# Optimization experiments

Measured on AMD Instinct MI355X. Metric: run time of the kernel, lower is better.

Reference implementation:

```python
import jax, jax.numpy as jnp
import numpy as np

HEADS = 8
WINDOW = 16

def _pointwise(W, b, t):
    # Conv1d(C, C, kernel=1): (B, C, T) -> (B, C, T)
    return jnp.einsum('oc,bct->bot', W, t) + b[None, :, None]

def setup_inputs() -> dict:
    key = jax.random.key(0)
    ks = jax.random.split(key, 10)
    B, C, T = 4, 512, 4096
    s = 0.02
    return {
        'x':    jax.random.normal(ks[0], (B, C, T), jnp.float32),
        'cond': jax.random.normal(ks[1], (B, C, T), jnp.float32),
        'Wq': jax.random.normal(ks[2], (C, C), jnp.float32) * s,
        'bq': jnp.zeros((C,), jnp.float32),
        'Wk': jax.random.normal(ks[3], (C, C), jnp.float32) * s,
        'bk': jnp.zeros((C,), jnp.float32),
        'Wv': jax.random.normal(ks[4], (C, C), jnp.float32) * s,
        'bv': jnp.zeros((C,), jnp.float32),
        'Wo': jax.random.normal(ks[5], (C, C), jnp.float32) * s,
        'bo': jnp.zeros((C,), jnp.float32),
    }

def reference(x, cond, Wq, bq, Wk, bk, Wv, bv, Wo, bo):
    B, C, T = x.shape
    H, W = HEADS, WINDOW
    hd = C // H
    scale = hd ** (-0.5)
    pad_left = W // 2          # 8
    pad_right = W - pad_left - 1  # 7

    q = _pointwise(Wq, bq, x)      # (B, C, T)
    k = _pointwise(Wk, bk, cond)
    v = _pointwise(Wv, bv, cond)

    k = jnp.pad(k, ((0, 0), (0, 0), (pad_left, pad_right)))  # (B, C, T+W-1)
    v = jnp.pad(v, ((0, 0), (0, 0), (pad_left, pad_right)))

    # sliding windows of size W, stride 1 -> T_unf == T
    idx = jnp.arange(T)[:, None] + jnp.arange(W)[None, :]  # (T, W)
    k_win = k[:, :, idx].reshape(B, H, hd, T, W)
    v_win = v[:, :, idx].reshape(B, H, hd, T, W)
    qh = q.reshape(B, H, hd, T)

    dots = jnp.einsum('bhdt,bhdtw->bhtw', qh, k_win) * scale
    attn = jax.nn.softmax(dots, axis=-1)
    out = jnp.einsum('bhtw,bhdtw->bhdt', attn, v_win)  # (B, H, hd, T)
    out = out.reshape(B, C, T)
    return _pointwise(Wo, bo, out)
```

## Files before the change

kernel.cpp:

```cpp
#include <hip/hip_runtime.h>

#define CC 512
#define TT 4096
#define NB 4
#define NH 8
#define HD 64

typedef __attribute__((ext_vector_type(8))) short s16x8;
typedef __attribute__((ext_vector_type(4))) float f32x4;
typedef __attribute__((ext_vector_type(4))) unsigned int u32x4;
typedef __attribute__((ext_vector_type(2))) unsigned int u32x2;

__device__ __forceinline__ short f2bf(float f) {
    unsigned u = __float_as_uint(f);
    unsigned r = (u + 0x7fffu + ((u >> 16) & 1u)) >> 16;
    return (short)r;
}
__device__ __forceinline__ unsigned pkbf(float a, float b) {
    return (unsigned)(unsigned short)f2bf(a) | ((unsigned)(unsigned short)f2bf(b) << 16);
}

__device__ __forceinline__ void gld_lds16(const void* g, void* s) {
    __builtin_amdgcn_global_load_lds(
        (const __attribute__((address_space(1))) unsigned int*)g,
        (__attribute__((address_space(3))) unsigned int*)s, 16, 0, 0);
}

__global__ __launch_bounds__(256) void cvt_w_k(const float* __restrict__ w0,
                                               const float* __restrict__ w1,
                                               const float* __restrict__ w2,
                                               const float* __restrict__ w3,
                                               short* __restrict__ dst) {
    int i = blockIdx.x * 256 + threadIdx.x;
    const float* s = (i < 262144) ? w0 : (i < 524288) ? w1 : (i < 786432) ? w2 : w3;
    dst[i] = f2bf(s[i & 262143]);
}

__global__ __launch_bounds__(256) void trans_k(const float* __restrict__ x,
                                               const float* __restrict__ cond,
                                               short* __restrict__ xT,
                                               short* __restrict__ condT) {
    __shared__ float tile[64][65];
    int z = blockIdx.z;
    int b = z & 3;
    const float* src = (z < 4 ? x : cond) + (size_t)b * CC * TT;
    short* dst = (z < 4 ? xT : condT) + (size_t)b * TT * CC;
    int tx = threadIdx.x & 63, ty = threadIdx.x >> 6;
    int t0 = blockIdx.x * 64, c0 = blockIdx.y * 64;
#pragma unroll
    for (int r = 0; r < 64; r += 4)
        tile[ty + r][tx] = src[(size_t)(c0 + ty + r) * TT + t0 + tx];
    __syncthreads();
#pragma unroll
    for (int r = 0; r < 64; r += 4)
        dst[(size_t)(t0 + ty + r) * CC + c0 + tx] = f2bf(tile[tx][ty + r]);
}

template <int OMODE>
__device__ __forceinline__ void gemm128(const short* __restrict__ Wm,
                                        const short* __restrict__ Sm,
                                        const float* __restrict__ bias,
                                        float* __restrict__ Df,
                                        short* __restrict__ Db) {
    __shared__ short Al[128 * 64] __attribute__((aligned(16)));
    __shared__ short Bl[128 * 64] __attribute__((aligned(16)));
    const int tid = threadIdx.x;
    const int lane = tid & 63;
    const int wid = tid >> 6;
    const int o0 = blockIdx.y * 128;
    const int t0 = blockIdx.x * 128;
    const int wm = (wid >> 1) * 64;
    const int wn = (wid & 1) * 64;

    f32x4 acc[4][4];
#pragma unroll
    for (int i = 0; i < 4; i++)
#pragma unroll
        for (int j = 0; j < 4; j++) acc[i][j] = (f32x4){0.f, 0.f, 0.f, 0.f};

    const int cbase = (wid * 4) << 6;

    for (int kt = 0; kt < 8; ++kt) {
        const int k0 = kt * 64;
        __syncthreads();
#pragma unroll
        for (int j = 0; j < 4; ++j) {
            int c = cbase + (j << 6) + lane;
            int m = c >> 3, kc = c & 7;
            int kcs = kc ^ (m & 7);
            gld_lds16(Wm + (size_t)(o0 + m) * CC + k0 + kcs * 8,
                      &Al[(cbase + (j << 6)) << 3]);
            gld_lds16(Sm + (size_t)(t0 + m) * CC + k0 + kcs * 8,
                      &Bl[(cbase + (j << 6)) << 3]);
        }
        __syncthreads();
#pragma unroll
        for (int kk = 0; kk < 2; ++kk) {
            const int kb = kk * 32 + (lane >> 4) * 8;
            s16x8 af[4], bfr[4];
#pragma unroll
            for (int i = 0; i < 4; i++) {
                int m = wm + i * 16 + (lane & 15);
                af[i] = *(const s16x8*)&Al[(m * 64 + kb) ^ ((m & 7) << 3)];
                int n = wn + i * 16 + (lane & 15);
                bfr[i] = *(const s16x8*)&Bl[(n * 64 + kb) ^ ((n & 7) << 3)];
            }
#pragma unroll
            for (int mi = 0; mi < 4; mi++)
#pragma unroll
                for (int ni = 0; ni < 4; ni++) {
                    if (OMODE == 1)
                        acc[mi][ni] = __builtin_amdgcn_mfma_f32_16x16x32_bf16(
                            bfr[mi], af[ni], acc[mi][ni], 0, 0, 0);
                    else
                        acc[mi][ni] = __builtin_amdgcn_mfma_f32_16x16x32_bf16(
                            af[mi], bfr[ni], acc[mi][ni], 0, 0, 0);
                }
        }
    }

    const int col = lane & 15;
    const int rg = (lane >> 4) << 2;
    if (OMODE == 1) {
#pragma unroll
        for (int ti = 0; ti < 4; ti++) {
            int t = t0 + wn + ti * 16 + rg;
#pragma unroll
            for (int oi = 0; oi < 4; oi++) {
                int o = o0 + wm + oi * 16 + col;
                float bv = bias[o];
                f32x4 a = acc[ti][oi];
#pragma unroll
                for (int r = 0; r < 4; r++)
                    Db[(size_t)(t + r) * CC + o] = f2bf(a[r] + bv);
            }
        }
    } else {
#pragma unroll
        for (int mi = 0; mi < 4; mi++) {
            int o = o0 + wm + mi * 16 + rg;
#pragma unroll
            for (int ni = 0; ni < 4; ni++) {
                int t = t0 + wn + ni * 16 + col;
                f32x4 a = acc[mi][ni];
#pragma unroll
                for (int r = 0; r < 4; r++) {
                    if (OMODE == 0)
                        Df[(size_t)(o + r) * TT + t] = a[r] + bias[o + r];
                    else
                        Db[(size_t)(o + r) * TT + t] = f2bf(a[r] + bias[o + r]);
                }
            }
        }
    }
}

__global__ __launch_bounds__(256, 2) void gemm_qkv_k(
    const short* __restrict__ Wb, const short* __restrict__ xT,
    const short* __restrict__ condT, const float* __restrict__ bq,
    const float* __restrict__ bk, const float* __restrict__ bv,
    short* __restrict__ qkvT) {
    int z = blockIdx.z, which = z >> 2, b = z & 3;
    const short* Wm = Wb + (size_t)which * CC * CC;
    const short* Sm = (which == 0 ? xT : condT) + (size_t)b * TT * CC;
    short* Db = qkvT + ((size_t)which * NB + b) * TT * CC;
    if (which == 2)
        gemm128<2>(Wm, Sm, bv, nullptr, Db);
    else
        gemm128<1>(Wm, Sm, which == 0 ? bq : bk, nullptr, Db);
}

__global__ __launch_bounds__(256, 2) void gemm_o_k(const short* __restrict__ Wb,
                                                   const short* __restrict__ outT,
                                                   const float* __restrict__ bo,
                                                   float* __restrict__ out) {
    int b = blockIdx.z;
    gemm128<0>(Wb + 3 * (size_t)CC * CC, outT + (size_t)b * TT * CC, bo,
               out + (size_t)b * CC * TT, nullptr);
}

__global__ __launch_bounds__(64, 4) void attn6_k(const short* __restrict__ qkvT,
                                                 short* __restrict__ outT) {
    __shared__ unsigned P_lds[2][16][18];
    const int lane = threadIdx.x;
    const int g = lane >> 4, tp = lane & 15;
    const int T0 = blockIdx.x * 32;
    const int h = blockIdx.y, b = blockIdx.z;
    const size_t BTC = (size_t)NB * TT * CC;
    const short* qg = qkvT + (size_t)b * TT * CC + h * HD;
    const short* kg = qg + BTC;
    const short* vg = qkvT + 2 * BTC + (size_t)b * TT * CC + (size_t)(h * HD) * TT;
    const f32x4 z4 = {0.f, 0.f, 0.f, 0.f};

    s16x8 ka0, ka1;
    {
        int s = T0 - 8 + tp;
        s = s < 0 ? 0 : s;
        const short* p = &kg[(size_t)s * CC + g * 8];
        ka0 = *(const s16x8*)p;
        ka1 = *(const s16x8*)(p + 32);
    }

#pragma unroll
    for (int m = 0; m < 2; ++m) {
        const int sb0 = T0 + 16 * m - 8;
        s16x8 kb0, kb1;
        {
            int s = sb0 + 16 + tp;
            s = s > TT - 1 ? TT - 1 : s;
            const short* p = &kg[(size_t)s * CC + g * 8];
            kb0 = *(const s16x8*)p;
            kb1 = *(const s16x8*)(p + 32);
        }
        s16x8 q0, q1;
        {
            const short* p = &qg[(size_t)(T0 + 16 * m + tp) * CC + g * 8];
            q0 = *(const s16x8*)p;
            q1 = *(const s16x8*)(p + 32);
        }
        int cb = sb0 + g * 8;
        cb = cb < 0 ? 0 : (cb > TT - 8 ? TT - 8 : cb);
        const short* vrow = &vg[(size_t)tp * TT + cb];
        s16x8 vf0 = *(const s16x8*)(vrow);
        s16x8 vf1 = *(const s16x8*)(vrow + (size_t)16 * TT);
        s16x8 vf2 = *(const s16x8*)(vrow + (size_t)32 * TT);
        s16x8 vf3 = *(const s16x8*)(vrow + (size_t)48 * TT);

        f32x4 s0 = __builtin_amdgcn_mfma_f32_16x16x32_bf16(ka0, q0, z4, 0, 0, 0);
        s0 = __builtin_amdgcn_mfma_f32_16x16x32_bf16(ka1, q1, s0, 0, 0, 0);
        f32x4 s1 = __builtin_amdgcn_mfma_f32_16x16x32_bf16(kb0, q0, z4, 0, 0, 0);
        s1 = __builtin_amdgcn_mfma_f32_16x16x32_bf16(kb1, q1, s1, 0, 0, 0);

        float lg[8];
        float mymax = -3.0e38f;
#pragma unroll
        for (int jr = 0; jr < 8; ++jr) {
            const int j = jr >> 2, r = jr & 3;
            float v = (j ? s1[r] : s0[r]) * 0.125f;
            const int sl = 16 * j + 4 * g + r;
            const int sg = sb0 + sl;
            v = ((unsigned)sg < (unsigned)TT) ? v : 0.f;
            lg[jr] = v;
            const bool inw = (unsigned)(sl - tp) < 16u;
            mymax = inw ? fmaxf(mymax, v) : mymax;
        }
        mymax = fmaxf(mymax, __shfl_xor(mymax, 16));
        mymax = fmaxf(mymax, __shfl_xor(mymax, 32));
        float e[8], Z = 0.f;
#pragma unroll
        for (int jr = 0; jr < 8; ++jr) {
            const int j = jr >> 2, r = jr & 3;
            const int sl = 16 * j + 4 * g + r;
            const bool inw = (unsigned)(sl - tp) < 16u;
            const float ee = inw ? __expf(lg[jr] - mymax) : 0.f;
            e[jr] = ee;
            Z += ee;
        }
        Z += __shfl_xor(Z, 16);
        Z += __shfl_xor(Z, 32);
        const float inv = 1.f / Z;
#pragma unroll
        for (int jr = 0; jr < 8; ++jr) {
            const int sg = sb0 + 16 * (jr >> 2) + 4 * g + (jr & 3);
            e[jr] = ((unsigned)sg < (unsigned)TT) ? e[jr] * inv : 0.f;
        }

        unsigned* prow = &P_lds[m & 1][tp][0];
        *(u32x2*)&prow[2 * g] = (u32x2){pkbf(e[0], e[1]), pkbf(e[2], e[3])};
        *(u32x2*)&prow[8 + 2 * g] = (u32x2){pkbf(e[4], e[5]), pkbf(e[6], e[7])};
        __syncthreads();
        const s16x8 pf = *(const s16x8*)&P_lds[m & 1][tp][4 * g];

        f32x4 o0 = __builtin_amdgcn_mfma_f32_16x16x32_bf16(vf0, pf, z4, 0, 0, 0);
        f32x4 o1 = __builtin_amdgcn_mfma_f32_16x16x32_bf16(vf1, pf, z4, 0, 0, 0);
        f32x4 o2 = __builtin_amdgcn_mfma_f32_16x16x32_bf16(vf2, pf, z4, 0, 0, 0);
        f32x4 o3 = __builtin_amdgcn_mfma_f32_16x16x32_bf16(vf3, pf, z4, 0, 0, 0);

        short* orow = &outT[((size_t)b * TT + T0 + 16 * m + tp) * CC + h * HD + 4 * g];
        *(u32x2*)&orow[0] = (u32x2){pkbf(o0[0], o0[1]), pkbf(o0[2], o0[3])};
        *(u32x2*)&orow[16] = (u32x2){pkbf(o1[0], o1[1]), pkbf(o1[2], o1[3])};
        *(u32x2*)&orow[32] = (u32x2){pkbf(o2[0], o2[1]), pkbf(o2[2], o2[3])};
        *(u32x2*)&orow[48] = (u32x2){pkbf(o3[0], o3[1]), pkbf(o3[2], o3[3])};

        ka0 = kb0;
        ka1 = kb1;
    }
}

extern "C" void kernel_launch(void* const* d_in, const int* in_sizes, int n_in,
                              void* d_out, int out_size, void* d_ws, size_t ws_size,
                              hipStream_t stream) {
    const float* x    = (const float*)d_in[0];
    const float* cond = (const float*)d_in[1];
    const float* Wq   = (const float*)d_in[2];
    const float* bq   = (const float*)d_in[3];
    const float* Wk   = (const float*)d_in[4];
    const float* bk   = (const float*)d_in[5];
    const float* Wv   = (const float*)d_in[6];
    const float* bv   = (const float*)d_in[7];
    const float* Wo   = (const float*)d_in[8];
    const float* bo   = (const float*)d_in[9];

    char* ws = (char*)d_ws;
    short* Wb    = (short*)ws;
    short* xT    = (short*)(ws + (2u << 20));
    short* condT = (short*)(ws + (18u << 20));
    short* qkvT  = (short*)(ws + (34u << 20));
    short* outT  = xT;

    cvt_w_k<<<4096, 256, 0, stream>>>(Wq, Wk, Wv, Wo, Wb);
    trans_k<<<dim3(TT / 64, CC / 64, 8), 256, 0, stream>>>(x, cond, xT, condT);
    gemm_qkv_k<<<dim3(TT / 128, CC / 128, 12), 256, 0, stream>>>(Wb, xT, condT, bq, bk, bv, qkvT);
    attn6_k<<<dim3(TT / 32, NH, NB), 64, 0, stream>>>(qkvT, outT);
    gemm_o_k<<<dim3(TT / 128, CC / 128, 4), 256, 0, stream>>>(Wb, outT, bo, (float*)d_out);
}
```

Before: 96.27 us.

## Enlarge GEMM tile to 256x128, load weights directly to registers, double-buffer activations

The shared GEMM routine now computes a 256-row output-channel by 128-token tile per block, with each wave owning a 128x64 sub-tile. Weight fragments are read from global memory straight into registers instead of being staged in LDS, on the expectation that the small weight matrix stays cached. The activation tile is double-buffered in LDS so the next K slice loads while MFMAs run on the current one, which drops one barrier per iteration. The trade-off is more accumulator registers per thread, half as many blocks in the grid, and uncoalesced per-lane global loads for the weights.

```diff
diff --git a/kernel.cpp b/kernel.cpp
--- a/kernel.cpp
+++ b/kernel.cpp
@@ -57,79 +57,92 @@
 }
 
 template <int OMODE>
-__device__ __forceinline__ void gemm128(const short* __restrict__ Wm,
+__device__ __forceinline__ void gemm256(const short* __restrict__ Wm,
                                         const short* __restrict__ Sm,
                                         const float* __restrict__ bias,
                                         float* __restrict__ Df,
                                         short* __restrict__ Db) {
-    __shared__ short Al[128 * 64] __attribute__((aligned(16)));
-    __shared__ short Bl[128 * 64] __attribute__((aligned(16)));
+    __shared__ short Bl[2][128 * 64] __attribute__((aligned(16)));
     const int tid = threadIdx.x;
     const int lane = tid & 63;
     const int wid = tid >> 6;
-    const int o0 = blockIdx.y * 128;
+    const int o0 = blockIdx.y * 256;
     const int t0 = blockIdx.x * 128;
-    const int wm = (wid >> 1) * 64;
+    const int wm = (wid >> 1) * 128;
     const int wn = (wid & 1) * 64;
 
-    f32x4 acc[4][4];
-#pragma unroll
-    for (int i = 0; i < 4; i++)
+    f32x4 acc[8][4];
+#pragma unroll
+    for (int i = 0; i < 8; i++)
 #pragma unroll
         for (int j = 0; j < 4; j++) acc[i][j] = (f32x4){0.f, 0.f, 0.f, 0.f};
 
-    const int cbase = (wid * 4) << 6;
+#define STAGE_B(BUF, K0)                                                     \
+    {                                                                        \
+        _Pragma("unroll") for (int it = 0; it < 4; ++it) {                   \
+            int idx = it * 256 + tid;                                        \
+            int row = idx >> 3, sl = idx & 7;                                \
+            int c = sl ^ (row & 7);                                          \
+            gld_lds16(Sm + (size_t)(t0 + row) * CC + (K0) + c * 8,           \
+                      &Bl[BUF][idx * 8]);                                    \
+        }                                                                    \
+    }
+
+    STAGE_B(0, 0);
+    __syncthreads();
 
     for (int kt = 0; kt < 8; ++kt) {
         const int k0 = kt * 64;
+        const int buf = kt & 1;
+
+        s16x8 af[2][8];
+        const short* abase =
+            Wm + (size_t)(o0 + wm + (lane & 15)) * CC + k0 + (lane >> 4) * 8;
+#pragma unroll
+        for (int ai = 0; ai < 8; ++ai) {
+            af[0][ai] = *(const s16x8*)(abase + (size_t)ai * 16 * CC);
+            af[1][ai] = *(const s16x8*)(abase + (size_t)ai * 16 * CC + 32);
+        }
+
+        if (kt < 7) STAGE_B(buf ^ 1, k0 + 64);
+
+#pragma unroll
+        for (int kk = 0; kk < 2; ++kk) {
+            s16x8 bfr[4];
+#pragma unroll
+            for (int bi = 0; bi < 4; ++bi) {
+                int n = wn + bi * 16 + (lane & 15);
+                bfr[bi] = *(const s16x8*)&Bl[buf][(n * 64 + kk * 32 +
+                                                   (lane >> 4) * 8) ^
+                                                  ((n & 7) << 3)];
+            }
+#pragma unroll
+            for (int ai = 0; ai < 8; ++ai)
+#pragma unroll
+                for (int bi = 0; bi < 4; ++bi) {
+                    if (OMODE == 1)
+                        acc[ai][bi] = __builtin_amdgcn_mfma_f32_16x16x32_bf16(
+                            bfr[bi], af[kk][ai], acc[ai][bi], 0, 0, 0);
+                    else
+                        acc[ai][bi] = __builtin_amdgcn_mfma_f32_16x16x32_bf16(
+                            af[kk][ai], bfr[bi], acc[ai][bi], 0, 0, 0);
+                }
+        }
         __syncthreads();
-#pragma unroll
-        for (int j = 0; j < 4; ++j) {
-            int c = cbase + (j << 6) + lane;
-            int m = c >> 3, kc = c & 7;
-            int kcs = kc ^ (m & 7);
-            gld_lds16(Wm + (size_t)(o0 + m) * CC + k0 + kcs * 8,
-                      &Al[(cbase + (j << 6)) << 3]);
-            gld_lds16(Sm + (size_t)(t0 + m) * CC + k0 + kcs * 8,
-                      &Bl[(cbase + (j << 6)) << 3]);
-        }
-        __syncthreads();
-#pragma unroll
-        for (int kk = 0; kk < 2; ++kk) {
-            const int kb = kk * 32 + (lane >> 4) * 8;
-            s16x8 af[4], bfr[4];
-#pragma unroll
-            for (int i = 0; i < 4; i++) {
-                int m = wm + i * 16 + (lane & 15);
-                af[i] = *(const s16x8*)&Al[(m * 64 + kb) ^ ((m & 7) << 3)];
-                int n = wn + i * 16 + (lane & 15);
-                bfr[i] = *(const s16x8*)&Bl[(n * 64 + kb) ^ ((n & 7) << 3)];
-            }
-#pragma unroll
-            for (int mi = 0; mi < 4; mi++)
-#pragma unroll
-                for (int ni = 0; ni < 4; ni++) {
-                    if (OMODE == 1)
-                        acc[mi][ni] = __builtin_amdgcn_mfma_f32_16x16x32_bf16(
-                            bfr[mi], af[ni], acc[mi][ni], 0, 0, 0);
-                    else
-                        acc[mi][ni] = __builtin_amdgcn_mfma_f32_16x16x32_bf16(
-                            af[mi], bfr[ni], acc[mi][ni], 0, 0, 0);
-                }
-        }
-    }
+    }
+#undef STAGE_B
 
     const int col = lane & 15;
     const int rg = (lane >> 4) << 2;
     if (OMODE == 1) {
 #pragma unroll
-        for (int ti = 0; ti < 4; ti++) {
-            int t = t0 + wn + ti * 16 + rg;
-#pragma unroll
-            for (int oi = 0; oi < 4; oi++) {
-                int o = o0 + wm + oi * 16 + col;
-                float bv = bias[o];
-                f32x4 a = acc[ti][oi];
+        for (int ai = 0; ai < 8; ++ai) {
+            int o = o0 + wm + ai * 16 + col;
+            float bv = bias[o];
+#pragma unroll
+            for (int bi = 0; bi < 4; ++bi) {
+                int t = t0 + wn + bi * 16 + rg;
+                f32x4 a = acc[ai][bi];
 #pragma unroll
                 for (int r = 0; r < 4; r++)
                     Db[(size_t)(t + r) * CC + o] = f2bf(a[r] + bv);
@@ -137,12 +150,12 @@
         }
     } else {
 #pragma unroll
-        for (int mi = 0; mi < 4; mi++) {
-            int o = o0 + wm + mi * 16 + rg;
-#pragma unroll
-            for (int ni = 0; ni < 4; ni++) {
-                int t = t0 + wn + ni * 16 + col;
-                f32x4 a = acc[mi][ni];
+        for (int ai = 0; ai < 8; ++ai) {
+            int o = o0 + wm + ai * 16 + rg;
+#pragma unroll
+            for (int bi = 0; bi < 4; ++bi) {
+                int t = t0 + wn + bi * 16 + col;
+                f32x4 a = acc[ai][bi];
 #pragma unroll
                 for (int r = 0; r < 4; r++) {
                     if (OMODE == 0)
@@ -165,9 +178,9 @@
     const short* Sm = (which == 0 ? xT : condT) + (size_t)b * TT * CC;
     short* Db = qkvT + ((size_t)which * NB + b) * TT * CC;
     if (which == 2)
-        gemm128<2>(Wm, Sm, bv, nullptr, Db);
+        gemm256<2>(Wm, Sm, bv, nullptr, Db);
     else
-        gemm128<1>(Wm, Sm, which == 0 ? bq : bk, nullptr, Db);
+        gemm256<1>(Wm, Sm, which == 0 ? bq : bk, nullptr, Db);
 }
 
 __global__ __launch_bounds__(256, 2) void gemm_o_k(const short* __restrict__ Wb,
@@ -175,7 +188,7 @@
                                                    const float* __restrict__ bo,
                                                    float* __restrict__ out) {
     int b = blockIdx.z;
-    gemm128<0>(Wb + 3 * (size_t)CC * CC, outT + (size_t)b * TT * CC, bo,
+    gemm256<0>(Wb + 3 * (size_t)CC * CC, outT + (size_t)b * TT * CC, bo,
                out + (size_t)b * CC * TT, nullptr);
 }
 
@@ -310,7 +323,7 @@
 
     cvt_w_k<<<4096, 256, 0, stream>>>(Wq, Wk, Wv, Wo, Wb);
     trans_k<<<dim3(TT / 64, CC / 64, 8), 256, 0, stream>>>(x, cond, xT, condT);
-    gemm_qkv_k<<<dim3(TT / 128, CC / 128, 12), 256, 0, stream>>>(Wb, xT, condT, bq, bk, bv, qkvT);
+    gemm_qkv_k<<<dim3(TT / 128, CC / 256, 12), 256, 0, stream>>>(Wb, xT, condT, bq, bk, bv, qkvT);
     attn6_k<<<dim3(TT / 32, NH, NB), 64, 0, stream>>>(qkvT, outT);
-    gemm_o_k<<<dim3(TT / 128, CC / 128, 4), 256, 0, stream>>>(Wb, outT, bo, (float*)d_out);
-}
+    gemm_o_k<<<dim3(TT / 128, CC / 256, 4), 256, 0, stream>>>(Wb, outT, bo, (float*)d_out);
+}
```

After: 141.6 us. +47.1%, slower.
